# Kernel optimization log

Hardware: AMD Instinct MI355X
Metric: run time of the kernel (lower is better)

The kernel has to match this reference:

```python
import jax, jax.numpy as jnp
import numpy as np

X_LIST = [256, 256, 1024, 1024, 512]
LABEL_DIM = 8
MAX_SEQ_LEN = 64
B = 256
EMB = 128
ATTR = 64
HID = 512
LAYERS = 4


def setup_inputs() -> dict:
    key = jax.random.key(0)
    ki = iter(jax.random.split(key, 80))
    def nrm(shape):
        return jax.random.normal(next(ki), shape, jnp.float32) * 0.02
    inp = {}
    inp['label'] = jax.random.normal(next(ki), (B, LABEL_DIM), jnp.float32)
    inp['length'] = jax.random.randint(next(ki), (B,), 1, MAX_SEQ_LEN + 1)
    inp['x'] = jnp.stack([jax.random.randint(next(ki), (B, MAX_SEQ_LEN), 0, v) for v in X_LIST], axis=-1)
    inp['x_now'] = jnp.stack([jax.random.randint(next(ki), (B, MAX_SEQ_LEN), 0, v) for v in X_LIST], axis=-1)
    for i, v in enumerate(X_LIST):
        inp[f'emb{i}'] = nrm((v, EMB))
    inp['pad_emb'] = jnp.zeros((1, ATTR), jnp.float32)
    for i in range(len(X_LIST) - 1):
        inp[f'cond_W{i}'] = nrm((ATTR, (i + 1) * EMB))
        inp[f'cond_b{i}'] = jnp.zeros((ATTR,), jnp.float32)
    inp['len_W'] = nrm((64, MAX_SEQ_LEN))
    inp['len_b'] = jnp.zeros((64,), jnp.float32)
    comb_in = EMB * len(X_LIST) + 64  # 704
    inp['comb_W'] = nrm((LABEL_DIM, HID, comb_in))
    inp['comb_b'] = jnp.zeros((LABEL_DIM, HID), jnp.float32)
    inp['lstm_Wih'] = nrm((LAYERS, 4 * HID, HID))
    inp['lstm_Whh'] = nrm((LAYERS, 4 * HID, HID))
    inp['lstm_bih'] = jnp.zeros((LAYERS, 4 * HID), jnp.float32)
    inp['lstm_bhh'] = jnp.zeros((LAYERS, 4 * HID), jnp.float32)
    for i, v in enumerate(X_LIST):
        inp[f'out_W{i}'] = nrm((v, HID + ATTR))
        inp[f'out_b{i}'] = jnp.zeros((v,), jnp.float32)
    return inp


def _forward(label, emb0, emb1, emb2, emb3, emb4, pad_emb,
             cond_W0, cond_W1, cond_W2, cond_W3, cond_b0, cond_b1, cond_b2, cond_b3,
             len_W, len_b, comb_W, comb_b,
             lstm_Wih, lstm_Whh, lstm_bih, lstm_bhh,
             out_W0, out_W1, out_W2, out_W3, out_W4,
             out_b0, out_b1, out_b2, out_b3, out_b4,
             length, x, x_now):
    embs = [emb0, emb1, emb2, emb3, emb4]
    cond_W = [cond_W0, cond_W1, cond_W2, cond_W3]
    cond_b = [cond_b0, cond_b1, cond_b2, cond_b3]
    out_W = [out_W0, out_W1, out_W2, out_W3, out_W4]
    out_b = [out_b0, out_b1, out_b2, out_b3, out_b4]
    Bn, T, _ = x.shape
    # length branch: one_hot(length-1) -> Linear -> ReLU -> [B, 64]
    length_oh = jax.nn.one_hot(length - 1, MAX_SEQ_LEN, dtype=jnp.float32)
    length_out = jax.nn.relu(length_oh @ len_W.T + len_b)
    # per-attribute embedding lookups, concat -> [B, T, 5*128]
    emb_list = jnp.concatenate([embs[i][x[:, :, i]] for i in range(len(X_LIST))], axis=2)
    now_emb = jnp.concatenate([embs[i][x_now[:, :, i]] for i in range(len(X_LIST) - 1)], axis=2)
    # condition features: pad for head 0, small MLPs on prefixes of now_emb
    attr = [jnp.broadcast_to(pad_emb, (Bn, T, ATTR))]
    for i in range(len(X_LIST) - 1):
        attr.append(jax.nn.relu(now_emb[:, :, :(i + 1) * EMB] @ cond_W[i].T + cond_b[i]))
    combined = jnp.concatenate(
        [emb_list, jnp.broadcast_to(length_out[:, None, :], (Bn, T, 64))], axis=2)  # [B,T,704]
    # label-routed combine_fc: compute all LABEL_DIM branches, gather matching branch
    fc = jax.nn.relu(jnp.einsum('btd,lhd->blth', combined, comb_W) + comb_b[None, :, None, :])
    label_int = jnp.argmax(label, axis=1)
    combined_out = jnp.take_along_axis(fc, label_int[:, None, None, None], axis=1)[:, 0]  # [B,T,H]
    # 4-layer LSTM, torch gate order (i,f,g,o), zero initial state
    xs = combined_out.transpose(1, 0, 2)  # [T,B,H]
    for l in range(LAYERS):
        Wih_T = lstm_Wih[l].T
        Whh_T = lstm_Whh[l].T
        bias = lstm_bih[l] + lstm_bhh[l]
        def step(carry, xt, Wih_T=Wih_T, Whh_T=Whh_T, bias=bias):
            h, c = carry
            g = xt @ Wih_T + h @ Whh_T + bias
            gi, gf, gg, go = jnp.split(g, 4, axis=-1)
            c = jax.nn.sigmoid(gf) * c + jax.nn.sigmoid(gi) * jnp.tanh(gg)
            h = jax.nn.sigmoid(go) * jnp.tanh(c)
            return (h, c), h
        z = jnp.zeros((Bn, HID), xs.dtype)
        _, xs = jax.lax.scan(step, (z, z), xs)
    hidden = xs.transpose(1, 0, 2)  # [B,T,H]
    # per-attribute log-softmax heads over [hidden ; attr_i]
    preds = [jax.nn.log_softmax(
        jnp.concatenate([hidden, attr[i]], axis=-1) @ out_W[i].T + out_b[i], axis=-1)
        for i in range(len(X_LIST))]
    return jnp.concatenate(preds, axis=-1)  # [B, T, sum(X_LIST)]


def reference(label, emb0, emb1, emb2, emb3, emb4, pad_emb,
              cond_W0, cond_W1, cond_W2, cond_W3, cond_b0, cond_b1, cond_b2, cond_b3,
              len_W, len_b, comb_W, comb_b,
              lstm_Wih, lstm_Whh, lstm_bih, lstm_bhh,
              out_W0, out_W1, out_W2, out_W3, out_W4,
              out_b0, out_b1, out_b2, out_b3, out_b4,
              length, x, x_now):
    return _forward(label, emb0, emb1, emb2, emb3, emb4, pad_emb,
                    cond_W0, cond_W1, cond_W2, cond_W3, cond_b0, cond_b1, cond_b2, cond_b3,
                    len_W, len_b, comb_W, comb_b,
                    lstm_Wih, lstm_Whh, lstm_bih, lstm_bhh,
                    out_W0, out_W1, out_W2, out_W3, out_W4,
                    out_b0, out_b1, out_b2, out_b3, out_b4,
                    length, x, x_now)
```

## Files before the change

### kernel.cpp

```cpp
#include <hip/hip_runtime.h>
#include <math.h>


#define B_    256
#define T_    64
#define EMB_  128
#define HID_  512
#define G4_   2048
#define CIN_  704
#define HA_   576
#define ROW_  3072
#define OFF_HA 2048
#define OFF_HB 2560

#define WKB_   516
#define WKC_   4128
#define HB0_   33024
#define SMEM_F 37120

#define BAR_T(tau) (64 + (tau) * 32)

struct Params {
  const float* label; const int* length; const int* x; const int* xnow;
  const float* emb[5]; const float* pad;
  const float* condW[4]; const float* condB[4];
  const float* lenW; const float* lenB;
  const float* combW; const float* combB;
  const float* Wih; const float* Whh; const float* bih; const float* bhh;
  const float* outW[5]; const float* outB[5];
  unsigned int* bar;
  float* out;
};

__device__ __forceinline__ void multi_barrier(unsigned int* cnt, unsigned int* gen,
                                              unsigned int n) {
  __syncthreads();
  if (threadIdx.x == 0) {
    unsigned int g = __hip_atomic_load(gen, __ATOMIC_RELAXED, __HIP_MEMORY_SCOPE_AGENT);
    unsigned int a = __hip_atomic_fetch_add(cnt, 1u, __ATOMIC_ACQ_REL, __HIP_MEMORY_SCOPE_AGENT);
    if (a == n - 1u) {
      __hip_atomic_store(cnt, 0u, __ATOMIC_RELAXED, __HIP_MEMORY_SCOPE_AGENT);
      __hip_atomic_store(gen, g + 1u, __ATOMIC_RELEASE, __HIP_MEMORY_SCOPE_AGENT);
    } else {
      while (__hip_atomic_load(gen, __ATOMIC_RELAXED, __HIP_MEMORY_SCOPE_AGENT) == g) {
        __builtin_amdgcn_s_sleep(2);
      }
      (void)__hip_atomic_load(gen, __ATOMIC_ACQUIRE, __HIP_MEMORY_SCOPE_AGENT);
    }
  }
  __syncthreads();
}

#define WRSLAB(SL) do { \
  _Pragma("unroll") \
  for (int qq = 0; qq < 16; ++qq) { \
    int cc = ((qq + lo) & 15) * 4; \
    *(float4*)&(SL)[lo * 64 + cc] = \
      make_float4(acc[qq >> 1][(qq & 1) * 4 + 0], acc[qq >> 1][(qq & 1) * 4 + 1], \
                  acc[qq >> 1][(qq & 1) * 4 + 2], acc[qq >> 1][(qq & 1) * 4 + 3]); \
  } } while (0)

#define RDSLAB(SL) do { \
  _Pragma("unroll") \
  for (int qq = 0; qq < 16; ++qq) { \
    int cc = ((qq + lo) & 15) * 4; \
    float4 vv = *(const float4*)&(SL)[lo * 64 + cc]; \
    acc[qq >> 1][(qq & 1) * 4 + 0] += vv.x; acc[qq >> 1][(qq & 1) * 4 + 1] += vv.y; \
    acc[qq >> 1][(qq & 1) * 4 + 2] += vv.z; acc[qq >> 1][(qq & 1) * 4 + 3] += vv.w; \
  } } while (0)

__global__ __launch_bounds__(256) void k_t1(Params P, int l) {
  __shared__ float sm[4608];
  const int out_off = (l & 1) ? OFF_HA : OFF_HB;
  const float* Wih = P.Wih + (size_t)l * G4_ * HID_;
  const int tid = threadIdx.x, blk = blockIdx.x;
  const int rt = blk >> 4, kt = blk & 15;
  const int r0 = rt * 128, k0 = kt * 32;
  const int ul = tid >> 3, kl = (tid & 7) * 4;
  #pragma unroll
  for (int p = 0; p < 4; ++p) {
    float4 v = *(const float4*)(Wih + (size_t)(r0 + p * 32 + ul) * HID_ + k0 + kl);
    *(float4*)&sm[(p * 32 + ul) * 36 + kl] = v;
  }
  __syncthreads();
  const int kk = tid >> 3, qb = (tid & 7) * 4;
  #pragma unroll
  for (int p = 0; p < 4; ++p) {
    int rl = qb + p * 32;
    float4 v = make_float4(sm[(rl + 0) * 36 + kk], sm[(rl + 1) * 36 + kk],
                           sm[(rl + 2) * 36 + kk], sm[(rl + 3) * 36 + kk]);
    int kabs = k0 + kk;
    int row = (r0 >> 8) * 256 + (kabs >> 1);
    int col = out_off + (kabs & 1) * 256 + (r0 & 255) + rl;
    *(float4*)&P.out[(size_t)row * ROW_ + col] = v;
  }
}

__global__ __launch_bounds__(256, 3) void k_gih(Params P, int l) {
  const int in_off  = (l & 1) ? OFF_HB : OFF_HA;
  const int out_off = (l & 1) ? OFF_HA : OFF_HB;
  const int tid = threadIdx.x;
  const int rg = tid & 63, mh = tid >> 6;
  const int rb = blockIdx.x >> 1, ch = blockIdx.x & 1;
  const int m_base = rb * 32;
  const float* arow[8];
  #pragma unroll
  for (int mm = 0; mm < 8; ++mm)
    arow[mm] = P.out + (size_t)(m_base + mh * 8 + mm) * ROW_ + in_off;
  for (int p0 = 0; p0 < 4; ++p0) {
    const int p = ch * 4 + p0;
    float acc[4][8];
    #pragma unroll
    for (int c = 0; c < 4; ++c)
      #pragma unroll
      for (int m = 0; m < 8; ++m) acc[c][m] = 0.f;
    const float* wp = P.out + (size_t)(p * 256) * ROW_ + out_off + rg * 4;
    for (int kq = 0; kq < 64; ++kq) {
      float4 w0 = *(const float4*)(wp);
      float4 w1 = *(const float4*)(wp + 256);
      float4 w2 = *(const float4*)(wp + ROW_);
      float4 w3 = *(const float4*)(wp + ROW_ + 256);
      #pragma unroll
      for (int mm = 0; mm < 8; ++mm) {
        float4 a = *(const float4*)(arow[mm] + kq * 4);
        acc[0][mm] += w0.x * a.x + w1.x * a.y + w2.x * a.z + w3.x * a.w;
        acc[1][mm] += w0.y * a.x + w1.y * a.y + w2.y * a.z + w3.y * a.w;
        acc[2][mm] += w0.z * a.x + w1.z * a.y + w2.z * a.z + w3.z * a.w;
        acc[3][mm] += w0.w * a.x + w1.w * a.y + w2.w * a.z + w3.w * a.w;
      }
      wp += 2 * ROW_;
    }
    int r4 = p * 256 + rg * 4;
    float4 bi = *(const float4*)(P.bih + l * G4_ + r4);
    float4 bh = *(const float4*)(P.bhh + l * G4_ + r4);
    float bx = bi.x + bh.x, by = bi.y + bh.y, bz = bi.z + bh.z, bw = bi.w + bh.w;
    #pragma unroll
    for (int mm = 0; mm < 8; ++mm) {
      int m = m_base + mh * 8 + mm;
      *(float4*)&P.out[(size_t)m * ROW_ + r4] =
        make_float4(acc[0][mm] + bx, acc[1][mm] + by,
                    acc[2][mm] + bz, acc[3][mm] + bw);
    }
  }
}

__global__ __launch_bounds__(256, 1) void k_lstmB(Params P, int l) {
  __shared__ float smem[SMEM_F];
  unsigned int* bar = P.bar;
  const int tid = threadIdx.x;
  const int blk = blockIdx.x;
  const int team = blk & 7, member = blk >> 3;
  const int out_off = (l & 1) ? OFF_HA : OFF_HB;

  const int kb  = tid >> 5;
  const int sgq = (tid >> 3) & 3;
  const int rg  = tid & 7;
  const bool owner = (tid < 32);
  const int s_base = team * 32 + sgq * 8;
  const int ucol0  = member * 16 + rg * 2;

  {
    const float* Wl = P.Whh + (size_t)l * G4_ * HID_;
    const int r = tid >> 2, q = tid & 3;
    const float* src = Wl + (size_t)((r & 3) * 512 + member * 16 + (r >> 2)) * HID_
                       + q * 128;
    for (int j = 0; j < 32; ++j) {
      float4 v = *(const float4*)(src + j * 4);
      int k0 = q * 128 + j * 4;
      #pragma unroll
      for (int e = 0; e < 4; ++e) {
        int k = k0 + e;
        smem[(k >> 6) * WKC_ + ((k >> 3) & 7) * WKB_ + (k & 7) * 64 + r] = (&v.x)[e];
      }
    }
  }
  __syncthreads();

  float cst[8][2];

  if (owner) {
    #pragma unroll
    for (int sj = 0; sj < 8; ++sj) {
      const size_t grow = (size_t)((s_base + sj) * 64 + 0) * ROW_;
      float2 zi2 = *(const float2*)&P.out[grow + 0 * 512 + ucol0];
      float2 zg2 = *(const float2*)&P.out[grow + 2 * 512 + ucol0];
      float2 zo2 = *(const float2*)&P.out[grow + 3 * 512 + ucol0];
      #pragma unroll
      for (int uj = 0; uj < 2; ++uj) {
        float zi = (&zi2.x)[uj], zg = (&zg2.x)[uj], zo = (&zo2.x)[uj];
        float si = 1.f / (1.f + expf(-zi));
        float so = 1.f / (1.f + expf(-zo));
        float cn = si * tanhf(zg);
        cst[sj][uj] = cn;
        P.out[grow + out_off + ucol0 + uj] = so * tanhf(cn);
      }
    }
  }

  for (int t = 1; t < T_; ++t) {
    multi_barrier(&bar[BAR_T(team)], &bar[BAR_T(team) + 16], 32);

    float Gp[8][4][2];
    if (owner) {
      #pragma unroll
      for (int sj = 0; sj < 8; ++sj) {
        const size_t grow = (size_t)((s_base + sj) * 64 + t) * ROW_;
        #pragma unroll
        for (int g = 0; g < 4; ++g) {
          float2 v = *(const float2*)&P.out[grow + g * 512 + ucol0];
          Gp[sj][g][0] = v.x; Gp[sj][g][1] = v.y;
        }
      }
    }

    float acc[8][8];
    #pragma unroll
    for (int a = 0; a < 8; ++a)
      #pragma unroll
      for (int b = 0; b < 8; ++b) acc[a][b] = 0.f;

    const int idx0 = tid * 2, idx1 = idx0 + 1;
    const int s0 = idx0 >> 4, kq0 = idx0 & 15;
    const int s1 = idx1 >> 4, kq1 = idx1 & 15;
    const size_t hrow0 = (size_t)((team * 32 + s0) * 64 + (t - 1)) * ROW_ + out_off;
    const size_t hrow1 = (size_t)((team * 32 + s1) * 64 + (t - 1)) * ROW_ + out_off;
    const int c0 = s0 * 64 + ((kq0 * 4 + 8 * (s0 >> 3)) & 63);
    const int c1 = s1 * 64 + ((kq1 * 4 + 8 * (s1 >> 3)) & 63);
    {
      float4 v0 = *(const float4*)&P.out[hrow0 + kq0 * 4];
      float4 v1 = *(const float4*)&P.out[hrow1 + kq1 * 4];
      *(float4*)&smem[HB0_ + c0] = v0;
      *(float4*)&smem[HB0_ + c1] = v1;
    }
    __syncthreads();

    for (int kc = 0; kc < 8; ++kc) {
      float4 nv0 = make_float4(0.f, 0.f, 0.f, 0.f), nv1 = nv0;
      if (kc < 7) {
        nv0 = *(const float4*)&P.out[hrow0 + (kc + 1) * 64 + kq0 * 4];
        nv1 = *(const float4*)&P.out[hrow1 + (kc + 1) * 64 + kq1 * 4];
      }
      const float* wp  = &smem[kc * WKC_ + kb * WKB_ + rg * 8];
      const float* hbv = &smem[HB0_ + (kc & 1) * 2048];
      #pragma unroll
      for (int kq2 = 0; kq2 < 2; ++kq2) {
        float4 h4[8];
        const int colr = kb * 8 + kq2 * 4;
        #pragma unroll
        for (int sj = 0; sj < 8; ++sj)
          h4[sj] = *(const float4*)&hbv[(sgq * 8 + sj) * 64 + ((colr + 8 * sgq) & 63)];
        #pragma unroll
        for (int e = 0; e < 4; ++e) {
          const float4 wA = *(const float4*)&wp[(kq2 * 4 + e) * 64];
          const float4 wB = *(const float4*)&wp[(kq2 * 4 + e) * 64 + 4];
          #pragma unroll
          for (int sj = 0; sj < 8; ++sj) {
            const float hv = (&h4[sj].x)[e];
            acc[sj][0] += hv * wA.x; acc[sj][1] += hv * wA.y;
            acc[sj][2] += hv * wA.z; acc[sj][3] += hv * wA.w;
            acc[sj][4] += hv * wB.x; acc[sj][5] += hv * wB.y;
            acc[sj][6] += hv * wB.z; acc[sj][7] += hv * wB.w;
          }
        }
      }
      if (kc < 7) {
        *(float4*)&smem[HB0_ + ((kc + 1) & 1) * 2048 + c0] = nv0;
        *(float4*)&smem[HB0_ + ((kc + 1) & 1) * 2048 + c1] = nv1;
      }
      __syncthreads();
    }

    #pragma unroll
    for (int a = 0; a < 8; ++a)
      #pragma unroll
      for (int b = 0; b < 8; ++b)
        acc[a][b] += __shfl_xor(acc[a][b], 32, 64);
    const int wv = tid >> 6;
    const bool halfLo = ((tid >> 5) & 1) == 0;
    const int lo = tid & 31;
    float* slab0 = &smem[HB0_];
    float* slab1 = &smem[HB0_ + 2048];
    if (halfLo && wv == 1) WRSLAB(slab0);
    if (halfLo && wv == 3) WRSLAB(slab1);
    __syncthreads();
    if (halfLo && wv == 0) RDSLAB(slab0);
    if (halfLo && wv == 2) RDSLAB(slab1);
    __syncthreads();
    if (halfLo && wv == 2) WRSLAB(slab0);
    __syncthreads();
    if (owner) {
      RDSLAB(slab0);
      #pragma unroll
      for (int sj = 0; sj < 8; ++sj) {
        const size_t orow = (size_t)((s_base + sj) * 64 + t) * ROW_;
        #pragma unroll
        for (int uj = 0; uj < 2; ++uj) {
          float zi = Gp[sj][0][uj] + acc[sj][uj * 4 + 0];
          float zf = Gp[sj][1][uj] + acc[sj][uj * 4 + 1];
          float zg = Gp[sj][2][uj] + acc[sj][uj * 4 + 2];
          float zo = Gp[sj][3][uj] + acc[sj][uj * 4 + 3];
          float si = 1.f / (1.f + expf(-zi));
          float sf = 1.f / (1.f + expf(-zf));
          float so = 1.f / (1.f + expf(-zo));
          float cn = sf * cst[sj][uj] + si * tanhf(zg);
          cst[sj][uj] = cn;
          P.out[orow + out_off + ucol0 + uj] = so * tanhf(cn);
        }
      }
    }
  }
}

__global__ __launch_bounds__(256) void k_combine(Params P) {
  __shared__ float sA[16][CIN_];
  __shared__ float sLen[64];
  int b = blockIdx.x >> 2, t0 = (blockIdx.x & 3) * 16;
  int tid = threadIdx.x;
  int li = P.length[b] - 1;
  if (tid < 64) {
    float v = P.lenW[tid * 64 + li] + P.lenB[tid];
    sLen[tid] = v > 0.f ? v : 0.f;
  }
  float best = P.label[b * 8]; int l = 0;
  #pragma unroll
  for (int k = 1; k < 8; ++k) {
    float lv = P.label[b * 8 + k];
    if (lv > best) { best = lv; l = k; }
  }
  __syncthreads();
  for (int tt = 0; tt < 16; ++tt) {
    int t = t0 + tt;
    for (int k = tid; k < CIN_; k += 256) {
      float v;
      if (k < 640) {
        int a = k >> 7, e = k & 127;
        int xi = P.x[((b * T_ + t) * 5) + a];
        v = P.emb[a][xi * EMB_ + e];
      } else {
        v = sLen[k - 640];
      }
      sA[tt][k] = v;
    }
  }
  __syncthreads();
  int hg = tid & 127, mh = tid >> 7;
  int h = hg * 4, tb = mh * 8;
  const float* W0 = P.combW + ((size_t)(l * HID_ + h)) * CIN_;
  float acc[4][8];
  #pragma unroll
  for (int c = 0; c < 4; ++c)
    #pragma unroll
    for (int m = 0; m < 8; ++m) acc[c][m] = 0.f;
  for (int k = 0; k < CIN_; k += 4) {
    float4 w0 = *(const float4*)(const void*)(W0 + k);
    float4 w1 = *(const float4*)(const void*)(W0 + CIN_ + k);
    float4 w2 = *(const float4*)(const void*)(W0 + 2 * CIN_ + k);
    float4 w3 = *(const float4*)(const void*)(W0 + 3 * CIN_ + k);
    #pragma unroll
    for (int m = 0; m < 8; ++m) {
      float4 av = *(const float4*)&sA[tb + m][k];
      acc[0][m] += w0.x*av.x + w0.y*av.y + w0.z*av.z + w0.w*av.w;
      acc[1][m] += w1.x*av.x + w1.y*av.y + w1.z*av.z + w1.w*av.w;
      acc[2][m] += w2.x*av.x + w2.y*av.y + w2.z*av.z + w2.w*av.w;
      acc[3][m] += w3.x*av.x + w3.y*av.y + w3.z*av.z + w3.w*av.w;
    }
  }
  #pragma unroll
  for (int c = 0; c < 4; ++c) {
    float bias = P.combB[l * HID_ + h + c];
    #pragma unroll
    for (int m = 0; m < 8; ++m) {
      float v = acc[c][m] + bias;
      P.out[((size_t)(b * T_ + t0 + tb + m)) * ROW_ + OFF_HA + h + c] = v > 0.f ? v : 0.f;
    }
  }
}

__global__ __launch_bounds__(256, 6) void k_heads(Params P) {
  __shared__ float sB[8][512];
  __shared__ float sAt[8][5][64];
  int m0 = blockIdx.x * 8;
  int tid = threadIdx.x;
  for (int i = tid; i < 8 * 512; i += 256) {
    int tt = i >> 9, k = i & 511;
    int a = k >> 7, e = k & 127;
    int xi = P.xnow[((m0 + tt) * 5) + a];
    sB[tt][k] = P.emb[a][xi * EMB_ + e];
  }
  for (int i = tid; i < 8 * 64; i += 256) {
    int tt = i >> 6, j = i & 63;
    sAt[tt][0][j] = P.pad[j];
  }
  __syncthreads();
  {
    int ih = tid >> 6, j = tid & 63;
    int Klen = (ih + 1) * EMB_;
    const float* Wr = P.condW[ih] + (size_t)j * Klen;
    float acc[8] = {0.f,0.f,0.f,0.f,0.f,0.f,0.f,0.f};
    for (int k = 0; k < Klen; k += 4) {
      float4 w = *(const float4*)(const void*)(Wr + k);
      #pragma unroll
      for (int m = 0; m < 8; ++m) {
        float4 av = *(const float4*)&sB[m][k];
        acc[m] += w.x*av.x + w.y*av.y + w.z*av.z + w.w*av.w;
      }
    }
    float bias = P.condB[ih][j];
    #pragma unroll
    for (int m = 0; m < 8; ++m) {
      float v = acc[m] + bias;
      sAt[m][ih + 1][j] = v > 0.f ? v : 0.f;
    }
  }
  __syncthreads();
  for (int i = tid; i < 8 * 512; i += 256) {
    int tt = i >> 9, k = i & 511;
    sB[tt][k] = P.out[((size_t)(m0 + tt)) * ROW_ + OFF_HA + k];
  }
  __syncthreads();
  const int V[5] = {256, 256, 1024, 1024, 512};
  int off = 0;
  int cg = tid & 127, mh = tid >> 7, tb = mh * 4;
  for (int head = 0; head < 5; ++head) {
    const float* W = P.outW[head];
    const float* bias = P.outB[head];
    int Vh = V[head];
    for (int c0 = cg * 4; c0 < Vh; c0 += 512) {
      const float* Wr = W + (size_t)c0 * HA_;
      float acc[4][4];
      #pragma unroll
      for (int c = 0; c < 4; ++c)
        #pragma unroll
        for (int m = 0; m < 4; ++m) acc[c][m] = 0.f;
      for (int k = 0; k < 512; k += 4) {
        float4 w0 = *(const float4*)(const void*)(Wr + k);
        float4 w1 = *(const float4*)(const void*)(Wr + HA_ + k);
        float4 w2 = *(const float4*)(const void*)(Wr + 2 * HA_ + k);
        float4 w3 = *(const float4*)(const void*)(Wr + 3 * HA_ + k);
        #pragma unroll
        for (int m = 0; m < 4; ++m) {
          float4 av = *(const float4*)&sB[tb + m][k];
          acc[0][m] += w0.x*av.x + w0.y*av.y + w0.z*av.z + w0.w*av.w;
          acc[1][m] += w1.x*av.x + w1.y*av.y + w1.z*av.z + w1.w*av.w;
          acc[2][m] += w2.x*av.x + w2.y*av.y + w2.z*av.z + w2.w*av.w;
          acc[3][m] += w3.x*av.x + w3.y*av.y + w3.z*av.z + w3.w*av.w;
        }
      }
      for (int k = 0; k < 64; k += 4) {
        float4 w0 = *(const float4*)(const void*)(Wr + 512 + k);
        float4 w1 = *(const float4*)(const void*)(Wr + HA_ + 512 + k);
        float4 w2 = *(const float4*)(const void*)(Wr + 2 * HA_ + 512 + k);
        float4 w3 = *(const float4*)(const void*)(Wr + 3 * HA_ + 512 + k);
        #pragma unroll
        for (int m = 0; m < 4; ++m) {
          float4 av = *(const float4*)&sAt[tb + m][head][k];
          acc[0][m] += w0.x*av.x + w0.y*av.y + w0.z*av.z + w0.w*av.w;
          acc[1][m] += w1.x*av.x + w1.y*av.y + w1.z*av.z + w1.w*av.w;
          acc[2][m] += w2.x*av.x + w2.y*av.y + w2.z*av.z + w2.w*av.w;
          acc[3][m] += w3.x*av.x + w3.y*av.y + w3.z*av.z + w3.w*av.w;
        }
      }
      #pragma unroll
      for (int c = 0; c < 4; ++c) {
        float bi = bias[c0 + c];
        #pragma unroll
        for (int m = 0; m < 4; ++m)
          P.out[((size_t)(m0 + tb + m)) * ROW_ + off + c0 + c] = acc[c][m] + bi;
      }
    }
    off += Vh;
  }
}

__global__ __launch_bounds__(256) void k_lsm(Params P) {
  __shared__ float sred[4];
  int m = blockIdx.x;
  float* row0 = P.out + (size_t)m * ROW_;
  int tid = threadIdx.x, lane = tid & 63, wid = tid >> 6;
  const int V[5] = {256, 256, 1024, 1024, 512};
  int off = 0;
  for (int head = 0; head < 5; ++head) {
    float* row = row0 + off; int Vh = V[head];
    float mx = -1e30f;
    for (int c = tid; c < Vh; c += 256) mx = fmaxf(mx, row[c]);
    for (int o = 32; o > 0; o >>= 1) mx = fmaxf(mx, __shfl_down(mx, o, 64));
    if (lane == 0) sred[wid] = mx;
    __syncthreads();
    mx = fmaxf(fmaxf(sred[0], sred[1]), fmaxf(sred[2], sred[3]));
    __syncthreads();
    float s = 0.f;
    for (int c = tid; c < Vh; c += 256) s += expf(row[c] - mx);
    for (int o = 32; o > 0; o >>= 1) s += __shfl_down(s, o, 64);
    if (lane == 0) sred[wid] = s;
    __syncthreads();
    float lse = mx + logf(sred[0] + sred[1] + sred[2] + sred[3]);
    __syncthreads();
    for (int c = tid; c < Vh; c += 256) row[c] = row[c] - lse;
    off += Vh;
  }
}

extern "C" void kernel_launch(void* const* d_in, const int* in_sizes, int n_in,
                              void* d_out, int out_size, void* d_ws, size_t ws_size,
                              hipStream_t stream) {
  (void)in_sizes; (void)n_in; (void)out_size; (void)ws_size;
  Params P;
  P.label  = (const float*)d_in[0];
  P.length = (const int*)  d_in[1];
  P.x      = (const int*)  d_in[2];
  P.xnow   = (const int*)  d_in[3];
  for (int i = 0; i < 5; ++i) P.emb[i] = (const float*)d_in[4 + i];
  P.pad = (const float*)d_in[9];
  for (int i = 0; i < 4; ++i) {
    P.condW[i] = (const float*)d_in[10 + 2 * i];
    P.condB[i] = (const float*)d_in[11 + 2 * i];
  }
  P.lenW  = (const float*)d_in[18]; P.lenB  = (const float*)d_in[19];
  P.combW = (const float*)d_in[20]; P.combB = (const float*)d_in[21];
  P.Wih   = (const float*)d_in[22]; P.Whh   = (const float*)d_in[23];
  P.bih   = (const float*)d_in[24]; P.bhh   = (const float*)d_in[25];
  for (int i = 0; i < 5; ++i) {
    P.outW[i] = (const float*)d_in[26 + 2 * i];
    P.outB[i] = (const float*)d_in[27 + 2 * i];
  }
  P.bar = (unsigned int*)d_ws;
  P.out = (float*)d_out;

  hipMemsetAsync(d_ws, 0, 1536, stream);
  k_combine<<<1024, 256, 0, stream>>>(P);
  for (int l = 0; l < 4; ++l) {
    k_t1 <<<256,  256, 0, stream>>>(P, l);
    k_gih<<<1024, 256, 0, stream>>>(P, l);
    void* args[] = { &P, &l };
    hipLaunchCooperativeKernel((void*)k_lstmB, dim3(256), dim3(256), args, 0, stream);
  }
  k_heads<<<2048,  256, 0, stream>>>(P);
  k_lsm  <<<16384, 256, 0, stream>>>(P);
}
```

Baseline: 14.28 ms.

## Split output heads into per-head templated kernels with 32-row tiles

Replaces the single k_heads kernel with one templated kernel per output head. Each block now processes 32 rows instead of 8, so every output-weight load is reused across four times as many rows. Each block computes only the conditional attribute projection its own head needs. Heads are launched so that head 3, which writes over the hidden-state region, runs last. The trade-off is more shared memory and registers per block, which lowers occupancy and adds four extra kernel launches.

```diff
diff --git a/kernel.cpp b/kernel.cpp
--- a/kernel.cpp
+++ b/kernel.cpp
@@ -376,99 +376,95 @@
   }
 }
 
-__global__ __launch_bounds__(256, 6) void k_heads(Params P) {
-  __shared__ float sB[8][512];
-  __shared__ float sAt[8][5][64];
-  int m0 = blockIdx.x * 8;
-  int tid = threadIdx.x;
-  for (int i = tid; i < 8 * 512; i += 256) {
-    int tt = i >> 9, k = i & 511;
-    int a = k >> 7, e = k & 127;
-    int xi = P.xnow[((m0 + tt) * 5) + a];
-    sB[tt][k] = P.emb[a][xi * EMB_ + e];
-  }
-  for (int i = tid; i < 8 * 64; i += 256) {
-    int tt = i >> 6, j = i & 63;
-    sAt[tt][0][j] = P.pad[j];
-  }
-  __syncthreads();
-  {
-    int ih = tid >> 6, j = tid & 63;
-    int Klen = (ih + 1) * EMB_;
-    const float* Wr = P.condW[ih] + (size_t)j * Klen;
+template<int HEAD, int VH, int OFF>
+__global__ __launch_bounds__(256, 2) void k_head(Params P) {
+  __shared__ float sB[32][512];
+  __shared__ float sAt[32][64];
+  const int tid = threadIdx.x;
+  const int m0 = blockIdx.x * 32;
+  if (HEAD == 0) {
+    for (int i = tid; i < 32 * 64; i += 256) sAt[i >> 6][i & 63] = P.pad[i & 63];
+  } else {
+    const int KA = HEAD * EMB_;
+    for (int i = tid; i < 32 * KA; i += 256) {
+      int tt = i / KA, k = i - tt * KA;
+      int a = k >> 7, e = k & 127;
+      int xi = P.xnow[((m0 + tt) * 5) + a];
+      sB[tt][k] = P.emb[a][xi * EMB_ + e];
+    }
+    __syncthreads();
+    int rg = tid >> 6, j = tid & 63;
+    const float* Wr = P.condW[HEAD - 1] + (size_t)j * KA;
     float acc[8] = {0.f,0.f,0.f,0.f,0.f,0.f,0.f,0.f};
-    for (int k = 0; k < Klen; k += 4) {
+    for (int k = 0; k < KA; k += 4) {
       float4 w = *(const float4*)(const void*)(Wr + k);
       #pragma unroll
       for (int m = 0; m < 8; ++m) {
-        float4 av = *(const float4*)&sB[m][k];
+        float4 av = *(const float4*)&sB[rg * 8 + m][k];
         acc[m] += w.x*av.x + w.y*av.y + w.z*av.z + w.w*av.w;
       }
     }
-    float bias = P.condB[ih][j];
+    float bias = P.condB[HEAD - 1][j];
     #pragma unroll
     for (int m = 0; m < 8; ++m) {
       float v = acc[m] + bias;
-      sAt[m][ih + 1][j] = v > 0.f ? v : 0.f;
-    }
-  }
-  __syncthreads();
-  for (int i = tid; i < 8 * 512; i += 256) {
+      sAt[rg * 8 + m][j] = v > 0.f ? v : 0.f;
+    }
+    __syncthreads();
+  }
+  for (int i = tid; i < 32 * 512; i += 256) {
     int tt = i >> 9, k = i & 511;
     sB[tt][k] = P.out[((size_t)(m0 + tt)) * ROW_ + OFF_HA + k];
   }
   __syncthreads();
-  const int V[5] = {256, 256, 1024, 1024, 512};
-  int off = 0;
-  int cg = tid & 127, mh = tid >> 7, tb = mh * 4;
-  for (int head = 0; head < 5; ++head) {
-    const float* W = P.outW[head];
-    const float* bias = P.outB[head];
-    int Vh = V[head];
-    for (int c0 = cg * 4; c0 < Vh; c0 += 512) {
-      const float* Wr = W + (size_t)c0 * HA_;
-      float acc[4][4];
-      #pragma unroll
-      for (int c = 0; c < 4; ++c)
-        #pragma unroll
-        for (int m = 0; m < 4; ++m) acc[c][m] = 0.f;
-      for (int k = 0; k < 512; k += 4) {
-        float4 w0 = *(const float4*)(const void*)(Wr + k);
-        float4 w1 = *(const float4*)(const void*)(Wr + HA_ + k);
-        float4 w2 = *(const float4*)(const void*)(Wr + 2 * HA_ + k);
-        float4 w3 = *(const float4*)(const void*)(Wr + 3 * HA_ + k);
-        #pragma unroll
-        for (int m = 0; m < 4; ++m) {
-          float4 av = *(const float4*)&sB[tb + m][k];
-          acc[0][m] += w0.x*av.x + w0.y*av.y + w0.z*av.z + w0.w*av.w;
-          acc[1][m] += w1.x*av.x + w1.y*av.y + w1.z*av.z + w1.w*av.w;
-          acc[2][m] += w2.x*av.x + w2.y*av.y + w2.z*av.z + w2.w*av.w;
-          acc[3][m] += w3.x*av.x + w3.y*av.y + w3.z*av.z + w3.w*av.w;
-        }
-      }
-      for (int k = 0; k < 64; k += 4) {
-        float4 w0 = *(const float4*)(const void*)(Wr + 512 + k);
-        float4 w1 = *(const float4*)(const void*)(Wr + HA_ + 512 + k);
-        float4 w2 = *(const float4*)(const void*)(Wr + 2 * HA_ + 512 + k);
-        float4 w3 = *(const float4*)(const void*)(Wr + 3 * HA_ + 512 + k);
-        #pragma unroll
-        for (int m = 0; m < 4; ++m) {
-          float4 av = *(const float4*)&sAt[tb + m][head][k];
-          acc[0][m] += w0.x*av.x + w0.y*av.y + w0.z*av.z + w0.w*av.w;
-          acc[1][m] += w1.x*av.x + w1.y*av.y + w1.z*av.z + w1.w*av.w;
-          acc[2][m] += w2.x*av.x + w2.y*av.y + w2.z*av.z + w2.w*av.w;
-          acc[3][m] += w3.x*av.x + w3.y*av.y + w3.z*av.z + w3.w*av.w;
-        }
-      }
-      #pragma unroll
-      for (int c = 0; c < 4; ++c) {
-        float bi = bias[c0 + c];
-        #pragma unroll
-        for (int m = 0; m < 4; ++m)
-          P.out[((size_t)(m0 + tb + m)) * ROW_ + off + c0 + c] = acc[c][m] + bi;
-      }
-    }
-    off += Vh;
+  constexpr int CG  = (VH >= 512) ? 128 : 64;
+  constexpr int RPG = (VH >= 512) ? 16 : 8;
+  const int cg = tid & (CG - 1), mh = tid / CG;
+  const int tb = mh * RPG;
+  const float* Wb = P.outW[HEAD];
+  const float* bs = P.outB[HEAD];
+  for (int c0 = cg * 4; c0 < VH; c0 += CG * 4) {
+    const float* Wr = Wb + (size_t)c0 * HA_;
+    float acc2[4][RPG];
+    #pragma unroll
+    for (int c = 0; c < 4; ++c)
+      #pragma unroll
+      for (int m = 0; m < RPG; ++m) acc2[c][m] = 0.f;
+    for (int k = 0; k < 512; k += 4) {
+      float4 w0 = *(const float4*)(const void*)(Wr + k);
+      float4 w1 = *(const float4*)(const void*)(Wr + HA_ + k);
+      float4 w2 = *(const float4*)(const void*)(Wr + 2 * HA_ + k);
+      float4 w3 = *(const float4*)(const void*)(Wr + 3 * HA_ + k);
+      #pragma unroll
+      for (int m = 0; m < RPG; ++m) {
+        float4 av = *(const float4*)&sB[tb + m][k];
+        acc2[0][m] += w0.x*av.x + w0.y*av.y + w0.z*av.z + w0.w*av.w;
+        acc2[1][m] += w1.x*av.x + w1.y*av.y + w1.z*av.z + w1.w*av.w;
+        acc2[2][m] += w2.x*av.x + w2.y*av.y + w2.z*av.z + w2.w*av.w;
+        acc2[3][m] += w3.x*av.x + w3.y*av.y + w3.z*av.z + w3.w*av.w;
+      }
+    }
+    for (int k = 0; k < 64; k += 4) {
+      float4 w0 = *(const float4*)(const void*)(Wr + 512 + k);
+      float4 w1 = *(const float4*)(const void*)(Wr + HA_ + 512 + k);
+      float4 w2 = *(const float4*)(const void*)(Wr + 2 * HA_ + 512 + k);
+      float4 w3 = *(const float4*)(const void*)(Wr + 3 * HA_ + 512 + k);
+      #pragma unroll
+      for (int m = 0; m < RPG; ++m) {
+        float4 av = *(const float4*)&sAt[tb + m][k];
+        acc2[0][m] += w0.x*av.x + w0.y*av.y + w0.z*av.z + w0.w*av.w;
+        acc2[1][m] += w1.x*av.x + w1.y*av.y + w1.z*av.z + w1.w*av.w;
+        acc2[2][m] += w2.x*av.x + w2.y*av.y + w2.z*av.z + w2.w*av.w;
+        acc2[3][m] += w3.x*av.x + w3.y*av.y + w3.z*av.z + w3.w*av.w;
+      }
+    }
+    #pragma unroll
+    for (int c = 0; c < 4; ++c) {
+      float bi = bs[c0 + c];
+      #pragma unroll
+      for (int m = 0; m < RPG; ++m)
+        P.out[((size_t)(m0 + tb + m)) * ROW_ + OFF + c0 + c] = acc2[c][m] + bi;
+    }
   }
 }
 
@@ -534,6 +530,10 @@
     void* args[] = { &P, &l };
     hipLaunchCooperativeKernel((void*)k_lstmB, dim3(256), dim3(256), args, 0, stream);
   }
-  k_heads<<<2048,  256, 0, stream>>>(P);
-  k_lsm  <<<16384, 256, 0, stream>>>(P);
-}
+  k_head<0,  256,    0><<<512, 256, 0, stream>>>(P);
+  k_head<1,  256,  256><<<512, 256, 0, stream>>>(P);
+  k_head<2, 1024,  512><<<512, 256, 0, stream>>>(P);
+  k_head<4,  512, 2560><<<512, 256, 0, stream>>>(P);
+  k_head<3, 1024, 1536><<<512, 256, 0, stream>>>(P);
+  k_lsm<<<16384, 256, 0, stream>>>(P);
+}
```

Result: faster. 11.85 ms (-17.0%).
